# Kernel tuning notes

Measured on AMD Instinct MI355X. Metric: run time of the kernel, lower is better.

## Reference

```python
import jax, jax.numpy as jnp
import numpy as np

HEAD_SIZE = 128
BLOCK_SIZE = 2048


def setup_inputs() -> dict:
    key = jax.random.key(0)
    k1, k2 = jax.random.split(key)
    B, T, D = 8, 2048, 1024
    x = jax.random.normal(k1, (B, T, D), dtype=jnp.float32)
    # Linear(dim, 3*head_size, bias=False): weight [3*head_size, dim], applied as x @ W.T
    W_qkv = jax.random.normal(k2, (3 * HEAD_SIZE, D), dtype=jnp.float32) * (1.0 / np.sqrt(D))
    return {"x": x, "W_qkv": W_qkv}


def reference(x, W_qkv):
    B, T, D = x.shape
    qkv = jnp.einsum('btd,hd->bth', x, W_qkv)  # [B, T, 3*head_size]
    q = qkv[:, :, :HEAD_SIZE]
    k = qkv[:, :, HEAD_SIZE:2 * HEAD_SIZE]
    v = qkv[:, :, 2 * HEAD_SIZE:]
    scale = 1.0 / np.sqrt(HEAD_SIZE).astype(np.float32)
    score = jnp.einsum('bqh,bkh->bqk', q, k) * scale  # [B, T, T]
    causal = jnp.tril(jnp.ones((T, T), dtype=bool))
    score = jnp.where(causal, score, -jnp.inf)
    attn = jax.nn.softmax(score, axis=-1)
    # dropout p=0.0 (eval) -> identity
    return jnp.einsum('bqk,bkh->bqh', attn, v)  # [B, T, head_size]
```

## Files before the change

### kernel.cpp

```cpp
#include <hip/hip_runtime.h>
#include <hip/hip_bf16.h>
#include <math.h>

#define D_MODEL 1024
#define TLEN    2048

typedef __attribute__((ext_vector_type(8))) short short8;
typedef __attribute__((ext_vector_type(4))) float f32x4;

static __device__ __forceinline__ unsigned short f2bf(float f) {
    __hip_bfloat16 h = __float2bfloat16(f);
    return __builtin_bit_cast(unsigned short, h);
}
static __device__ __forceinline__ float bf2f(unsigned short u) {
    unsigned int x = ((unsigned int)u) << 16;
    return __builtin_bit_cast(float, x);
}
static __device__ __forceinline__ void lds_cp16(void* lds, const void* g) {
    __builtin_amdgcn_global_load_lds(
        (const __attribute__((address_space(1))) unsigned int*)g,
        (__attribute__((address_space(3))) unsigned int*)lds, 16, 0, 0);
}

__global__ __launch_bounds__(256) void pack_w(const float* __restrict__ W,
                                              unsigned short* __restrict__ wt) {
    const int id = blockIdx.x * 256 + threadIdx.x;
    const int h  = id >> 7;
    const int kg = id & 127;
    const int k0 = kg * 8;
    const int kt = k0 >> 6;
    const int kin = k0 & 63;
    const int np = h >> 7;
    const int hp = h & 127;
    const float4 a = *(const float4*)&W[(size_t)h * D_MODEL + k0];
    const float4 b = *(const float4*)&W[(size_t)h * D_MODEL + k0 + 4];
    short8 v;
    v[0] = (short)f2bf(a.x); v[1] = (short)f2bf(a.y);
    v[2] = (short)f2bf(a.z); v[3] = (short)f2bf(a.w);
    v[4] = (short)f2bf(b.x); v[5] = (short)f2bf(b.y);
    v[6] = (short)f2bf(b.z); v[7] = (short)f2bf(b.w);
    const size_t dst = ((size_t)(np * 16 + kt) * 128 + hp) * 64 + (kin ^ ((hp & 7) * 8));
    *(short8*)&wt[dst] = v;
}

__global__ __launch_bounds__(256, 4) void qkv_gemm(const float* __restrict__ x,
                                                   const unsigned short* __restrict__ wt,
                                                   unsigned short* __restrict__ qk,
                                                   unsigned short* __restrict__ vt) {
    __shared__ unsigned short As[64][88];
    __shared__ unsigned short Bs[128 * 64];

    const int tid  = threadIdx.x;
    const int lane = tid & 63;
    const int w    = tid >> 6;
    const int wm   = w >> 1, wn = w & 1;
    const int cc   = lane & 15, g = lane >> 4;
    const int row0 = blockIdx.x * 64;
    const int np   = blockIdx.y;

    const int xr  = tid >> 2;
    const int xc0 = (tid & 3) * 16;

    const f32x4 zero = {0.f, 0.f, 0.f, 0.f};
    f32x4 acc[2][4];
#pragma unroll
    for (int i = 0; i < 2; ++i)
#pragma unroll
        for (int j = 0; j < 4; ++j) acc[i][j] = zero;

    const float* xrow = x + (size_t)(row0 + xr) * D_MODEL + xc0;
    float4 xa[4];
#pragma unroll
    for (int i = 0; i < 4; ++i) xa[i] = *(const float4*)(xrow + i * 4);

    const unsigned short* wtile0 =
        wt + (size_t)np * 16 * 128 * 64 + (w * 4 * 1024 + lane * 16) / 2;
    unsigned short* bdst = Bs + (w * 4 * 1024) / 2;

    for (int kt = 0; kt < 16; ++kt) {
        __syncthreads();
        {
            short8 s0, s1;
            s0[0] = (short)f2bf(xa[0].x); s0[1] = (short)f2bf(xa[0].y);
            s0[2] = (short)f2bf(xa[0].z); s0[3] = (short)f2bf(xa[0].w);
            s0[4] = (short)f2bf(xa[1].x); s0[5] = (short)f2bf(xa[1].y);
            s0[6] = (short)f2bf(xa[1].z); s0[7] = (short)f2bf(xa[1].w);
            s1[0] = (short)f2bf(xa[2].x); s1[1] = (short)f2bf(xa[2].y);
            s1[2] = (short)f2bf(xa[2].z); s1[3] = (short)f2bf(xa[2].w);
            s1[4] = (short)f2bf(xa[3].x); s1[5] = (short)f2bf(xa[3].y);
            s1[6] = (short)f2bf(xa[3].z); s1[7] = (short)f2bf(xa[3].w);
            *(short8*)&As[xr][xc0]     = s0;
            *(short8*)&As[xr][xc0 + 8] = s1;
        }
        const unsigned short* wtk = wtile0 + (size_t)kt * 128 * 64;
#pragma unroll
        for (int i = 0; i < 4; ++i)
            lds_cp16(bdst + i * 512, wtk + i * 512);
        __syncthreads();

        short8 af[2][2], bf[2][4];
#pragma unroll
        for (int ks = 0; ks < 2; ++ks) {
#pragma unroll
            for (int mt = 0; mt < 2; ++mt)
                af[ks][mt] = *(const short8*)&As[wm * 32 + mt * 16 + cc][ks * 32 + g * 8];
#pragma unroll
            for (int nt = 0; nt < 4; ++nt) {
                const int h = wn * 64 + nt * 16 + cc;
                bf[ks][nt] = *(const short8*)&Bs[h * 64 + (((ks * 4 + g) ^ (h & 7)) << 3)];
            }
        }
        if (kt + 1 < 16) {
#pragma unroll
            for (int i = 0; i < 4; ++i)
                xa[i] = *(const float4*)(xrow + (kt + 1) * 64 + i * 4);
        }
#pragma unroll
        for (int ks = 0; ks < 2; ++ks)
#pragma unroll
            for (int mt = 0; mt < 2; ++mt)
#pragma unroll
                for (int nt = 0; nt < 4; ++nt)
                    acc[mt][nt] = __builtin_amdgcn_mfma_f32_16x16x32_bf16(
                        af[ks][mt], bf[ks][nt], acc[mt][nt], 0, 0, 0);
    }

    const int bb  = row0 >> 11;
    const int tr0 = row0 & 2047;
    const float qs = (np == 0) ? 0.08838834764831845f : 1.0f;
#pragma unroll
    for (int mt = 0; mt < 2; ++mt)
#pragma unroll
        for (int nt = 0; nt < 4; ++nt) {
            const int colp = wn * 64 + nt * 16;
            if (np < 2) {
#pragma unroll
                for (int r = 0; r < 4; ++r) {
                    const int row = row0 + wm * 32 + mt * 16 + g * 4 + r;
                    qk[(size_t)row * 256 + np * 128 + colp + cc] = f2bf(acc[mt][nt][r] * qs);
                }
            } else {
                const int d    = colp + cc;
                const int trow = tr0 + wm * 32 + mt * 16 + g * 4;
                ushort4 u;
                u.x = f2bf(acc[mt][nt][0]);
                u.y = f2bf(acc[mt][nt][1]);
                u.z = f2bf(acc[mt][nt][2]);
                u.w = f2bf(acc[mt][nt][3]);
                *(ushort4*)&vt[((size_t)(bb * 128 + d)) * TLEN + trow] = u;
            }
        }
}

__global__ __launch_bounds__(256, 3) void attn_part(const unsigned short* __restrict__ qk,
                                                    const unsigned short* __restrict__ vt,
                                                    unsigned short* __restrict__ po,
                                                    float2* __restrict__ ml) {
    __shared__ unsigned short Ks[64 * 128];
    __shared__ unsigned short Vs[128 * 64];
    __shared__ unsigned short Ps[4][16][72];

    const int tid  = threadIdx.x;
    const int lane = tid & 63;
    const int w    = tid >> 6;
    const int cc   = lane & 15, g = lane >> 4;
    const int bx   = blockIdx.x;
    const int qt   = 31 - (bx / 3);
    const int ggg  = bx % 3;
    const int b    = blockIdx.y;
    const int q0   = qt * 64;
    const int slot = (b * 32 + qt) * 3 + ggg;
    const int n    = qt + 1;
    const int cnt  = (n > ggg) ? ((n - ggg + 2) / 3) : 0;

    if (cnt == 0) {
#pragma unroll
        for (int nt = 0; nt < 8; ++nt)
#pragma unroll
            for (int r = 0; r < 4; ++r)
                po[((size_t)slot * 64 + w * 16 + g * 4 + r) * 128 + nt * 16 + cc] = 0;
        if (g == 0) ml[slot * 64 + w * 16 + cc] = make_float2(-INFINITY, 0.f);
        return;
    }

    short8 qf[4];
    {
        const unsigned short* qb =
            qk + ((size_t)(b * TLEN + q0 + w * 16 + cc)) * 256 + g * 8;
#pragma unroll
        for (int kt = 0; kt < 4; ++kt) qf[kt] = *(const short8*)(qb + kt * 32);
    }

    const f32x4 zero = {0.f, 0.f, 0.f, 0.f};
    f32x4 o[8];
#pragma unroll
    for (int nt = 0; nt < 8; ++nt) o[nt] = zero;
    float mrun = -INFINITY, lrun = 0.f;

    int koff[4], voff[2];
#pragma unroll
    for (int kt = 0; kt < 4; ++kt)
        koff[kt] = cc * 128 + (((kt * 4 + g) ^ (cc & 7)) << 3);
#pragma unroll
    for (int ks = 0; ks < 2; ++ks)
        voff[ks] = cc * 64 + (((ks * 4 + g) ^ (cc & 7)) << 3);

    const int kRow = tid >> 2;
    const int kG0  = (tid & 3) * 4;
    const int vRow = tid >> 1;
    const int vG0  = (tid & 1) * 4;
    const unsigned short* kgp = qk + ((size_t)(b * TLEN + kRow)) * 256 + 128 + kG0 * 8;
    const unsigned short* vgp = vt + ((size_t)(b * 128 + vRow)) * TLEN + vG0 * 8;

    short8 kr[4], vr[4];
#pragma unroll
    for (int i = 0; i < 4; ++i) kr[i] = *(const short8*)(kgp + (size_t)ggg * 16384 + i * 8);
#pragma unroll
    for (int i = 0; i < 4; ++i) vr[i] = *(const short8*)(vgp + ggg * 64 + i * 8);

    for (int s = 0; s < cnt; ++s) {
        const int t  = 3 * s + ggg;
        const int j0 = t * 64;
        __syncthreads();
#pragma unroll
        for (int i = 0; i < 4; ++i) {
            *(short8*)&Ks[kRow * 128 + (((kG0 + i) ^ (kRow & 7)) << 3)] = kr[i];
            *(short8*)&Vs[vRow * 64  + (((vG0 + i) ^ (vRow & 7)) << 3)] = vr[i];
        }
        __syncthreads();
        if (s + 1 < cnt) {
            const int tn = t + 3;
#pragma unroll
            for (int i = 0; i < 4; ++i) kr[i] = *(const short8*)(kgp + (size_t)tn * 16384 + i * 8);
#pragma unroll
            for (int i = 0; i < 4; ++i) vr[i] = *(const short8*)(vgp + tn * 64 + i * 8);
        }

        f32x4 st[4];
#pragma unroll
        for (int jt = 0; jt < 4; ++jt) st[jt] = zero;
        __builtin_amdgcn_s_setprio(1);
#pragma unroll
        for (int kt = 0; kt < 4; ++kt)
#pragma unroll
            for (int jt = 0; jt < 4; ++jt) {
                const short8 kf = *(const short8*)&Ks[koff[kt] + jt * 2048];
                st[jt] = __builtin_amdgcn_mfma_f32_16x16x32_bf16(kf, qf[kt], st[jt], 0, 0, 0);
            }
        __builtin_amdgcn_s_setprio(0);

        if (t == qt) {
            const int qg = q0 + w * 16 + cc;
            const int jb = j0 + 4 * g;
#pragma unroll
            for (int jt = 0; jt < 4; ++jt)
#pragma unroll
                for (int r = 0; r < 4; ++r)
                    if (jb + jt * 16 + r > qg) st[jt][r] = -INFINITY;
        }
        float pmax = -INFINITY;
#pragma unroll
        for (int jt = 0; jt < 4; ++jt) {
            const float a = fmaxf(st[jt][0], st[jt][1]);
            const float c = fmaxf(st[jt][2], st[jt][3]);
            pmax = fmaxf(pmax, fmaxf(a, c));
        }
        pmax = fmaxf(pmax, __shfl_xor(pmax, 16));
        pmax = fmaxf(pmax, __shfl_xor(pmax, 32));

        if (!__all(pmax <= mrun + 8.f)) {
            const float newm  = fmaxf(mrun, pmax);
            const float alpha = __expf(mrun - newm);
            mrun = newm;
            lrun *= alpha;
            float arow[4];
#pragma unroll
            for (int r = 0; r < 4; ++r) arow[r] = __shfl(alpha, 20 * g + r);
#pragma unroll
            for (int nt = 0; nt < 8; ++nt)
#pragma unroll
                for (int r = 0; r < 4; ++r) o[nt][r] *= arow[r];
        }

        float rs = 0.f;
#pragma unroll
        for (int jt = 0; jt < 4; ++jt) {
            const float p0 = __expf(st[jt][0] - mrun);
            const float p1 = __expf(st[jt][1] - mrun);
            const float p2 = __expf(st[jt][2] - mrun);
            const float p3 = __expf(st[jt][3] - mrun);
            rs += (p0 + p1) + (p2 + p3);
            uint2 pw;
            pw.x = (unsigned int)f2bf(p0) | ((unsigned int)f2bf(p1) << 16);
            pw.y = (unsigned int)f2bf(p2) | ((unsigned int)f2bf(p3) << 16);
            *(uint2*)&Ps[w][cc][jt * 16 + 4 * g] = pw;
        }
        rs += __shfl_xor(rs, 16);
        rs += __shfl_xor(rs, 32);
        lrun += rs;

        asm volatile("s_waitcnt lgkmcnt(0)" ::: "memory");
        __builtin_amdgcn_sched_barrier(0);

        __builtin_amdgcn_s_setprio(1);
#pragma unroll
        for (int ks = 0; ks < 2; ++ks) {
            const short8 pa = *(const short8*)&Ps[w][cc][ks * 32 + g * 8];
#pragma unroll
            for (int nt = 0; nt < 8; ++nt) {
                const short8 vf = *(const short8*)&Vs[voff[ks] + nt * 1024];
                o[nt] = __builtin_amdgcn_mfma_f32_16x16x32_bf16(pa, vf, o[nt], 0, 0, 0);
            }
        }
        __builtin_amdgcn_s_setprio(0);
    }

#pragma unroll
    for (int nt = 0; nt < 8; ++nt)
#pragma unroll
        for (int r = 0; r < 4; ++r)
            po[((size_t)slot * 64 + w * 16 + g * 4 + r) * 128 + nt * 16 + cc] =
                f2bf(o[nt][r]);
    if (g == 0) ml[slot * 64 + w * 16 + cc] = make_float2(mrun, lrun);
}

__global__ __launch_bounds__(256) void attn_merge(const unsigned short* __restrict__ po,
                                                  const float2* __restrict__ ml,
                                                  float* __restrict__ out) {
    const int bq   = blockIdx.x;
    const int row  = threadIdx.x >> 2;
    const int cs   = (threadIdx.x & 3) * 32;
    const int slot = bq * 3;

    const float2 ml0 = ml[(size_t)(slot + 0) * 64 + row];
    const float2 ml1 = ml[(size_t)(slot + 1) * 64 + row];
    const float2 ml2 = ml[(size_t)(slot + 2) * 64 + row];
    const float M  = fmaxf(fmaxf(ml0.x, ml1.x), ml2.x);
    float e0 = __expf(ml0.x - M);
    float e1 = __expf(ml1.x - M);
    float e2 = __expf(ml2.x - M);
    const float inv = 1.f / (ml0.y * e0 + ml1.y * e1 + ml2.y * e2);
    e0 *= inv; e1 *= inv; e2 *= inv;

    const unsigned short* p0 = po + ((size_t)(slot + 0) * 64 + row) * 128 + cs;
    const unsigned short* p1 = po + ((size_t)(slot + 1) * 64 + row) * 128 + cs;
    const unsigned short* p2 = po + ((size_t)(slot + 2) * 64 + row) * 128 + cs;
    float* op = out + ((size_t)bq * 64 + row) * 128 + cs;

#pragma unroll
    for (int i = 0; i < 4; ++i) {
        const short8 a = *(const short8*)(p0 + i * 8);
        const short8 b = *(const short8*)(p1 + i * 8);
        const short8 c = *(const short8*)(p2 + i * 8);
        float4 o0, o1;
        o0.x = bf2f((unsigned short)a[0]) * e0 + bf2f((unsigned short)b[0]) * e1 + bf2f((unsigned short)c[0]) * e2;
        o0.y = bf2f((unsigned short)a[1]) * e0 + bf2f((unsigned short)b[1]) * e1 + bf2f((unsigned short)c[1]) * e2;
        o0.z = bf2f((unsigned short)a[2]) * e0 + bf2f((unsigned short)b[2]) * e1 + bf2f((unsigned short)c[2]) * e2;
        o0.w = bf2f((unsigned short)a[3]) * e0 + bf2f((unsigned short)b[3]) * e1 + bf2f((unsigned short)c[3]) * e2;
        o1.x = bf2f((unsigned short)a[4]) * e0 + bf2f((unsigned short)b[4]) * e1 + bf2f((unsigned short)c[4]) * e2;
        o1.y = bf2f((unsigned short)a[5]) * e0 + bf2f((unsigned short)b[5]) * e1 + bf2f((unsigned short)c[5]) * e2;
        o1.z = bf2f((unsigned short)a[6]) * e0 + bf2f((unsigned short)b[6]) * e1 + bf2f((unsigned short)c[6]) * e2;
        o1.w = bf2f((unsigned short)a[7]) * e0 + bf2f((unsigned short)b[7]) * e1 + bf2f((unsigned short)c[7]) * e2;
        *(float4*)(op + i * 8)     = o0;
        *(float4*)(op + i * 8 + 4) = o1;
    }
}

extern "C" void kernel_launch(void* const* d_in, const int* in_sizes, int n_in,
                              void* d_out, int out_size, void* d_ws, size_t ws_size,
                              hipStream_t stream) {
    (void)in_sizes; (void)n_in; (void)out_size; (void)ws_size;
    const float* x = (const float*)d_in[0];
    const float* W = (const float*)d_in[1];
    float* out = (float*)d_out;

    unsigned short* qkbf = (unsigned short*)d_ws;
    unsigned short* vtbf = qkbf + (size_t)16384 * 256;
    unsigned short* wtbf = vtbf + (size_t)8 * 128 * 2048;
    unsigned short* pobf = wtbf + (size_t)3 * 16 * 128 * 64;
    float2*         mlf  = (float2*)(pobf + (size_t)768 * 64 * 128);

    pack_w<<<dim3(192), 256, 0, stream>>>(W, wtbf);
    qkv_gemm<<<dim3(256, 3), 256, 0, stream>>>(x, wtbf, qkbf, vtbf);
    attn_part<<<dim3(96, 8), 256, 0, stream>>>(qkbf, vtbf, pobf, mlf);
    attn_merge<<<dim3(256), 256, 0, stream>>>(pobf, mlf, out);
}
```

Baseline: 68.90 us.

## Compute all QKV columns per block so x is read and converted once

The QKV GEMM now uses 32-row tiles with all 384 output columns per block, instead of 64 rows by 128 columns across three grid slices. Each fp32 x row is therefore loaded and converted to bf16 once rather than three times, which cuts the dominant x traffic. The weight packing is relaid out as one 384-wide k-tile, the A tile gets an XOR swizzle, and MFMA sections raise wave priority with s_setprio. In exchange each block holds a larger LDS footprint and more accumulators, so occupancy drops to 2 blocks per CU, and it reloads the full 384x64 weight tile per k-step.

```diff
diff --git a/kernel.cpp b/kernel.cpp
--- a/kernel.cpp
+++ b/kernel.cpp
@@ -30,8 +30,6 @@
     const int k0 = kg * 8;
     const int kt = k0 >> 6;
     const int kin = k0 & 63;
-    const int np = h >> 7;
-    const int hp = h & 127;
     const float4 a = *(const float4*)&W[(size_t)h * D_MODEL + k0];
     const float4 b = *(const float4*)&W[(size_t)h * D_MODEL + k0 + 4];
     short8 v;
@@ -39,109 +37,105 @@
     v[2] = (short)f2bf(a.z); v[3] = (short)f2bf(a.w);
     v[4] = (short)f2bf(b.x); v[5] = (short)f2bf(b.y);
     v[6] = (short)f2bf(b.z); v[7] = (short)f2bf(b.w);
-    const size_t dst = ((size_t)(np * 16 + kt) * 128 + hp) * 64 + (kin ^ ((hp & 7) * 8));
+    const size_t dst = ((size_t)kt * 384 + h) * 64 + (kin ^ ((h & 7) * 8));
     *(short8*)&wt[dst] = v;
 }
 
-__global__ __launch_bounds__(256, 4) void qkv_gemm(const float* __restrict__ x,
+__global__ __launch_bounds__(256, 2) void qkv_gemm(const float* __restrict__ x,
                                                    const unsigned short* __restrict__ wt,
                                                    unsigned short* __restrict__ qk,
                                                    unsigned short* __restrict__ vt) {
-    __shared__ unsigned short As[64][88];
-    __shared__ unsigned short Bs[128 * 64];
+    __shared__ unsigned short As[32 * 64];
+    __shared__ unsigned short Bs[384 * 64];
 
     const int tid  = threadIdx.x;
     const int lane = tid & 63;
     const int w    = tid >> 6;
-    const int wm   = w >> 1, wn = w & 1;
     const int cc   = lane & 15, g = lane >> 4;
-    const int row0 = blockIdx.x * 64;
-    const int np   = blockIdx.y;
-
-    const int xr  = tid >> 2;
-    const int xc0 = (tid & 3) * 16;
+    const int row0 = blockIdx.x * 32;
+
+    const int xr  = tid >> 3;
+    const int xg  = tid & 7;
 
     const f32x4 zero = {0.f, 0.f, 0.f, 0.f};
-    f32x4 acc[2][4];
+    f32x4 acc[2][6];
 #pragma unroll
     for (int i = 0; i < 2; ++i)
 #pragma unroll
-        for (int j = 0; j < 4; ++j) acc[i][j] = zero;
-
-    const float* xrow = x + (size_t)(row0 + xr) * D_MODEL + xc0;
-    float4 xa[4];
-#pragma unroll
-    for (int i = 0; i < 4; ++i) xa[i] = *(const float4*)(xrow + i * 4);
-
-    const unsigned short* wtile0 =
-        wt + (size_t)np * 16 * 128 * 64 + (w * 4 * 1024 + lane * 16) / 2;
-    unsigned short* bdst = Bs + (w * 4 * 1024) / 2;
+        for (int j = 0; j < 6; ++j) acc[i][j] = zero;
+
+    const float* xrow = x + (size_t)(row0 + xr) * D_MODEL + xg * 8;
+    float4 xa0 = *(const float4*)(xrow);
+    float4 xa1 = *(const float4*)(xrow + 4);
+
+    const unsigned short* wsrc0 = wt + w * 6144 + lane * 8;
+    unsigned short* bdst = Bs + w * 6144;
+
+    const int aw = xr * 64 + ((xg ^ (xr & 7)) << 3);
 
     for (int kt = 0; kt < 16; ++kt) {
         __syncthreads();
         {
-            short8 s0, s1;
-            s0[0] = (short)f2bf(xa[0].x); s0[1] = (short)f2bf(xa[0].y);
-            s0[2] = (short)f2bf(xa[0].z); s0[3] = (short)f2bf(xa[0].w);
-            s0[4] = (short)f2bf(xa[1].x); s0[5] = (short)f2bf(xa[1].y);
-            s0[6] = (short)f2bf(xa[1].z); s0[7] = (short)f2bf(xa[1].w);
-            s1[0] = (short)f2bf(xa[2].x); s1[1] = (short)f2bf(xa[2].y);
-            s1[2] = (short)f2bf(xa[2].z); s1[3] = (short)f2bf(xa[2].w);
-            s1[4] = (short)f2bf(xa[3].x); s1[5] = (short)f2bf(xa[3].y);
-            s1[6] = (short)f2bf(xa[3].z); s1[7] = (short)f2bf(xa[3].w);
-            *(short8*)&As[xr][xc0]     = s0;
-            *(short8*)&As[xr][xc0 + 8] = s1;
-        }
-        const unsigned short* wtk = wtile0 + (size_t)kt * 128 * 64;
-#pragma unroll
-        for (int i = 0; i < 4; ++i)
+            short8 s0;
+            s0[0] = (short)f2bf(xa0.x); s0[1] = (short)f2bf(xa0.y);
+            s0[2] = (short)f2bf(xa0.z); s0[3] = (short)f2bf(xa0.w);
+            s0[4] = (short)f2bf(xa1.x); s0[5] = (short)f2bf(xa1.y);
+            s0[6] = (short)f2bf(xa1.z); s0[7] = (short)f2bf(xa1.w);
+            *(short8*)&As[aw] = s0;
+        }
+        const unsigned short* wtk = wsrc0 + (size_t)kt * 24576;
+#pragma unroll
+        for (int i = 0; i < 12; ++i)
             lds_cp16(bdst + i * 512, wtk + i * 512);
         __syncthreads();
 
-        short8 af[2][2], bf[2][4];
+        short8 af[2][2], bf[2][6];
 #pragma unroll
         for (int ks = 0; ks < 2; ++ks) {
 #pragma unroll
+            for (int mt = 0; mt < 2; ++mt) {
+                const int row = mt * 16 + cc;
+                af[ks][mt] = *(const short8*)&As[row * 64 + (((ks * 4 + g) ^ (row & 7)) << 3)];
+            }
+#pragma unroll
+            for (int nt = 0; nt < 6; ++nt) {
+                const int h = w * 96 + nt * 16 + cc;
+                bf[ks][nt] = *(const short8*)&Bs[h * 64 + (((ks * 4 + g) ^ (h & 7)) << 3)];
+            }
+        }
+        if (kt + 1 < 16) {
+            xa0 = *(const float4*)(xrow + (kt + 1) * 64);
+            xa1 = *(const float4*)(xrow + (kt + 1) * 64 + 4);
+        }
+        __builtin_amdgcn_s_setprio(1);
+#pragma unroll
+        for (int ks = 0; ks < 2; ++ks)
+#pragma unroll
             for (int mt = 0; mt < 2; ++mt)
-                af[ks][mt] = *(const short8*)&As[wm * 32 + mt * 16 + cc][ks * 32 + g * 8];
-#pragma unroll
-            for (int nt = 0; nt < 4; ++nt) {
-                const int h = wn * 64 + nt * 16 + cc;
-                bf[ks][nt] = *(const short8*)&Bs[h * 64 + (((ks * 4 + g) ^ (h & 7)) << 3)];
-            }
-        }
-        if (kt + 1 < 16) {
-#pragma unroll
-            for (int i = 0; i < 4; ++i)
-                xa[i] = *(const float4*)(xrow + (kt + 1) * 64 + i * 4);
-        }
-#pragma unroll
-        for (int ks = 0; ks < 2; ++ks)
-#pragma unroll
-            for (int mt = 0; mt < 2; ++mt)
-#pragma unroll
-                for (int nt = 0; nt < 4; ++nt)
+#pragma unroll
+                for (int nt = 0; nt < 6; ++nt)
                     acc[mt][nt] = __builtin_amdgcn_mfma_f32_16x16x32_bf16(
                         af[ks][mt], bf[ks][nt], acc[mt][nt], 0, 0, 0);
+        __builtin_amdgcn_s_setprio(0);
     }
 
     const int bb  = row0 >> 11;
     const int tr0 = row0 & 2047;
-    const float qs = (np == 0) ? 0.08838834764831845f : 1.0f;
 #pragma unroll
     for (int mt = 0; mt < 2; ++mt)
 #pragma unroll
-        for (int nt = 0; nt < 4; ++nt) {
-            const int colp = wn * 64 + nt * 16;
-            if (np < 2) {
+        for (int nt = 0; nt < 6; ++nt) {
+            const int h = w * 96 + nt * 16 + cc;
+            if (h < 256) {
+                const float qs = (h < 128) ? 0.08838834764831845f : 1.0f;
 #pragma unroll
                 for (int r = 0; r < 4; ++r) {
-                    const int row = row0 + wm * 32 + mt * 16 + g * 4 + r;
-                    qk[(size_t)row * 256 + np * 128 + colp + cc] = f2bf(acc[mt][nt][r] * qs);
+                    const int row = row0 + mt * 16 + g * 4 + r;
+                    qk[(size_t)row * 256 + h] = f2bf(acc[mt][nt][r] * qs);
                 }
             } else {
-                const int d    = colp + cc;
-                const int trow = tr0 + wm * 32 + mt * 16 + g * 4;
+                const int d    = h - 256;
+                const int trow = tr0 + mt * 16 + g * 4;
                 ushort4 u;
                 u.x = f2bf(acc[mt][nt][0]);
                 u.y = f2bf(acc[mt][nt][1]);
@@ -377,11 +371,11 @@
     unsigned short* qkbf = (unsigned short*)d_ws;
     unsigned short* vtbf = qkbf + (size_t)16384 * 256;
     unsigned short* wtbf = vtbf + (size_t)8 * 128 * 2048;
-    unsigned short* pobf = wtbf + (size_t)3 * 16 * 128 * 64;
+    unsigned short* pobf = wtbf + (size_t)16 * 384 * 64;
     float2*         mlf  = (float2*)(pobf + (size_t)768 * 64 * 128);
 
     pack_w<<<dim3(192), 256, 0, stream>>>(W, wtbf);
-    qkv_gemm<<<dim3(256, 3), 256, 0, stream>>>(x, wtbf, qkbf, vtbf);
+    qkv_gemm<<<dim3(512), 256, 0, stream>>>(x, wtbf, qkbf, vtbf);
     attn_part<<<dim3(96, 8), 256, 0, stream>>>(qkbf, vtbf, pobf, mlf);
     attn_merge<<<dim3(256), 256, 0, stream>>>(pobf, mlf, out);
 }
```

After: 70.34 us. 1.02x slower.
